# Optimization experiments

Measured on AMD Instinct MI355X. Metric: run time of the kernel, lower is better.

The kernel has to match this reference:

```python
import jax, jax.numpy as jnp
import numpy as np

OUT_DIM = 4096
DPC = 16
N = OUT_DIM * DPC  # 65536
BATCH = 512


def setup_inputs() -> dict:
    key = jax.random.key(0)
    k1, k2 = jax.random.split(key)
    x = jax.random.normal(k1, (BATCH, N), dtype=jnp.float32)
    duty_cycle = jax.random.uniform(k2, (N,), dtype=jnp.float32)
    boost_strength = jnp.ones((1,), dtype=jnp.float32)
    return {"x": x, "duty_cycle": duty_cycle, "boost_strength": boost_strength}


def reference(x, duty_cycle, boost_strength):
    # GenericKWinners.forward in training mode (k = out_dim), boost_strength > 0.
    n = x.shape[1]
    target_density = OUT_DIM / n
    bs = boost_strength[0]
    boost_factors = jnp.exp((target_density - duty_cycle) * bs)  # [N]
    # x is detached in the original before boosting/masking
    boosted = jax.lax.stop_gradient(x) * boost_factors  # [B, N]
    # Overlapping windows: group k covers [k*(dpc-1), k*(dpc-1)+dpc)
    starts = jnp.arange(OUT_DIM) * (DPC - 1)  # [OUT_DIM]
    win_idx = starts[:, None] + jnp.arange(DPC)[None, :]  # [OUT_DIM, DPC]
    windows = boosted[:, win_idx]  # [B, OUT_DIM, DPC]
    ind = jnp.argmax(windows, axis=-1)  # [B, OUT_DIM]
    mask = jax.nn.one_hot(ind, DPC, dtype=x.dtype)  # [B, OUT_DIM, DPC]
    mask = mask.reshape(x.shape[0], OUT_DIM * DPC)  # [B, N]
    return mask * x
```

## Files before the change

### kernel.cpp

```cpp
#include <hip/hip_runtime.h>

#define OUT_DIM 4096
#define DPC     16
#define NCOL    65536
#define BATCH   512
#define TOTAL_W (BATCH * OUT_DIM)

__global__ void boost_table_kernel(const float* __restrict__ duty,
                                   const float* __restrict__ bs_ptr,
                                   float* __restrict__ bf) {
    int p = blockIdx.x * blockDim.x + threadIdx.x;
    if (p < NCOL) {
        float t = (0.0625f - duty[p]) * bs_ptr[0];
        bf[p] = (float)exp((double)t);
    }
}

__global__ __launch_bounds__(256) void dkw_kernel(const float* __restrict__ x,
                                                  const float* __restrict__ bf,
                                                  float* __restrict__ out) {
    const int lane = threadIdx.x & 63;
    const int wave = threadIdx.x >> 6;
    const int j    = lane & 15;
    const int sub  = lane >> 4;
    const unsigned inv_j = 15u - (unsigned)j;

    int W = (blockIdx.x * 4 + wave) * 4 + sub;
    const int strideW = gridDim.x * 16;

    for (; W < TOTAL_W; W += strideW) {
        const int b = W >> 12;
        const int w = W & 4095;
        const int rowbase = b << 16;

        const int col_in = w * 15 + j;
        float v   = x[rowbase + col_in];
        float bfv = bf[col_in];
        float boosted = v * bfv;

        unsigned ub  = __float_as_uint(boosted);
        unsigned ord = ((int)ub < 0) ? ~ub : (ub | 0x80000000u);
        unsigned long long key = ((unsigned long long)ord << 4) | inv_j;

        #pragma unroll
        for (int m = 1; m <= 8; m <<= 1) {
            unsigned long long other =
                (unsigned long long)__shfl_xor((long long)key, m);
            if (other > key) key = other;
        }
        const int jstar = 15 - (int)(key & 15ull);

        const int oidx = rowbase + (w << 4) + j;
        float xo = x[oidx];
        out[oidx] = (j == jstar) ? xo : 0.0f;
    }
}

extern "C" void kernel_launch(void* const* d_in, const int* in_sizes, int n_in,
                              void* d_out, int out_size, void* d_ws, size_t ws_size,
                              hipStream_t stream) {
    const float* x    = (const float*)d_in[0];
    const float* duty = (const float*)d_in[1];
    const float* bs   = (const float*)d_in[2];
    float* out = (float*)d_out;
    float* bf  = (float*)d_ws;

    hipLaunchKernelGGL(boost_table_kernel, dim3(NCOL / 256), dim3(256), 0, stream,
                       duty, bs, bf);
    hipLaunchKernelGGL(dkw_kernel, dim3(4096), dim3(256), 0, stream,
                       x, bf, out);
}
```

Baseline: 247.2 us.

## Stage boosted window span in LDS and vectorize loads and stores

Each block now handles 512 windows of one row. It loads the overlapping input span with float4 into shared memory, multiplies by the boost factors there, and each thread picks the argmax for two windows with a serial scan instead of wave shuffles. The output is then written with float4 loads and stores using a shared jstar table. This is meant to cut the per-element scalar global loads and the 64-bit shuffle reductions, at the cost of LDS traffic, likely bank conflicts from the stride-15 window reads, and two barriers per block.

```diff
diff --git a/kernel.cpp b/kernel.cpp
--- a/kernel.cpp
+++ b/kernel.cpp
@@ -4,7 +4,9 @@
 #define DPC     16
 #define NCOL    65536
 #define BATCH   512
-#define TOTAL_W (BATCH * OUT_DIM)
+#define WPB     512
+#define SPAN    7681
+#define SPAN_F4 1921
 
 __global__ void boost_table_kernel(const float* __restrict__ duty,
                                    const float* __restrict__ bs_ptr,
@@ -19,40 +21,58 @@
 __global__ __launch_bounds__(256) void dkw_kernel(const float* __restrict__ x,
                                                   const float* __restrict__ bf,
                                                   float* __restrict__ out) {
-    const int lane = threadIdx.x & 63;
-    const int wave = threadIdx.x >> 6;
-    const int j    = lane & 15;
-    const int sub  = lane >> 4;
-    const unsigned inv_j = 15u - (unsigned)j;
+    __shared__ float s_boost[SPAN_F4 * 4];
+    __shared__ int   s_jstar[WPB];
 
-    int W = (blockIdx.x * 4 + wave) * 4 + sub;
-    const int strideW = gridDim.x * 16;
+    const int tid = threadIdx.x;
+    const int row = blockIdx.x >> 3;
+    const int w0  = (blockIdx.x & 7) * WPB;
+    const int rowbase = row << 16;
 
-    for (; W < TOTAL_W; W += strideW) {
-        const int b = W >> 12;
-        const int w = W & 4095;
-        const int rowbase = b << 16;
+    const int in_off = w0 * 15;
+    const float4* __restrict__ xg = (const float4*)(x + rowbase + in_off);
+    const float4* __restrict__ bg = (const float4*)(bf + in_off);
+    float4* __restrict__ sb4 = (float4*)s_boost;
+    #pragma unroll
+    for (int i = tid; i < SPAN_F4; i += 256) {
+        float4 a = xg[i];
+        float4 b = bg[i];
+        float4 p;
+        p.x = a.x * b.x; p.y = a.y * b.y; p.z = a.z * b.z; p.w = a.w * b.w;
+        sb4[i] = p;
+    }
+    __syncthreads();
 
-        const int col_in = w * 15 + j;
-        float v   = x[rowbase + col_in];
-        float bfv = bf[col_in];
-        float boosted = v * bfv;
+    #pragma unroll
+    for (int r = 0; r < 2; ++r) {
+        const int w = tid + r * 256;
+        const float* __restrict__ p = s_boost + w * 15;
+        float best = p[0];
+        int   bj   = 0;
+        #pragma unroll
+        for (int k = 1; k < DPC; ++k) {
+            float v = p[k];
+            if (v > best) { best = v; bj = k; }
+        }
+        s_jstar[w] = bj;
+    }
+    __syncthreads();
 
-        unsigned ub  = __float_as_uint(boosted);
-        unsigned ord = ((int)ub < 0) ? ~ub : (ub | 0x80000000u);
-        unsigned long long key = ((unsigned long long)ord << 4) | inv_j;
-
-        #pragma unroll
-        for (int m = 1; m <= 8; m <<= 1) {
-            unsigned long long other =
-                (unsigned long long)__shfl_xor((long long)key, m);
-            if (other > key) key = other;
-        }
-        const int jstar = 15 - (int)(key & 15ull);
-
-        const int oidx = rowbase + (w << 4) + j;
-        float xo = x[oidx];
-        out[oidx] = (j == jstar) ? xo : 0.0f;
+    const int out_off = rowbase + (w0 << 4);
+    const float4* __restrict__ xo = (const float4*)(x + out_off);
+    float4* __restrict__ og = (float4*)(out + out_off);
+    #pragma unroll
+    for (int i = tid; i < (WPB * DPC) / 4; i += 256) {
+        float4 v = xo[i];
+        const int w  = i >> 2;
+        const int jm = s_jstar[w];
+        const int j  = (i & 3) << 2;
+        float4 o;
+        o.x = (j     == jm) ? v.x : 0.0f;
+        o.y = (j + 1 == jm) ? v.y : 0.0f;
+        o.z = (j + 2 == jm) ? v.z : 0.0f;
+        o.w = (j + 3 == jm) ? v.w : 0.0f;
+        og[i] = o;
     }
 }
 
@@ -67,6 +87,6 @@
 
     hipLaunchKernelGGL(boost_table_kernel, dim3(NCOL / 256), dim3(256), 0, stream,
                        duty, bs, bf);
-    hipLaunchKernelGGL(dkw_kernel, dim3(4096), dim3(256), 0, stream,
+    hipLaunchKernelGGL(dkw_kernel, dim3(BATCH * 8), dim3(256), 0, stream,
                        x, bf, out);
 }
```

Measured after the change: 249.1 us. About the same (+0.8%).
